# Kernel tuning notes

Measured on AMD Instinct MI355X. Metric: run time of the kernel, lower is better.

## Reference

```python
import jax, jax.numpy as jnp
import numpy as np

N, E, F_IN, F_OUT = 8192, 1024, 256, 256


def setup_inputs() -> dict:
    key = jax.random.key(0)
    k1, k2, k3, k4 = jax.random.split(key, 4)
    X = jax.random.normal(k1, (N, F_IN), dtype=jnp.float32)
    # binary incidence matrix: node i belongs to hyperedge j with p=0.05
    H = (jax.random.uniform(k2, (N, E)) < 0.05).astype(jnp.float32)
    W = jax.random.normal(k3, (F_OUT, F_IN), dtype=jnp.float32) * (1.0 / np.sqrt(F_IN))
    b = jax.random.normal(k4, (F_OUT,), dtype=jnp.float32) * 0.01
    return {"X": X, "H": H, "W": W, "b": b}


def reference(X, H, W, b):
    # Dv = diag(row sums of H), De = diag(col sums of H)
    dv = jnp.sum(H, axis=1)                      # [N] node degrees
    de = jnp.sum(H, axis=0)                      # [E] edge degrees
    dv_inv_sqrt = 1.0 / jnp.sqrt(dv)             # inv of sqrt(Dv) (diagonal)
    de_inv = 1.0 / de                            # inv of De (diagonal)
    # diagonal matrices realized as broadcast scalings (same math, no N x N).
    Xs = X * dv_inv_sqrt[:, None]
    M = H.T @ Xs                                 # H^T (...)          [E, F]
    M = M * de_inv[:, None]                      # De^-1 (...)        [E, F]
    X_new = (H @ M) * dv_inv_sqrt[:, None]       # Dv^-1/2 H (...)    [N, F]
    return X_new @ W.T + b                       # nn.Linear
```

## Files before the change

### kernel.cpp

```cpp
#include <hip/hip_runtime.h>
#include <hip/hip_bf16.h>
#include <stdint.h>

typedef __attribute__((ext_vector_type(8))) short bf16x8;
typedef __attribute__((ext_vector_type(4))) float f32x4;
typedef __attribute__((ext_vector_type(4))) unsigned int u32x4;
typedef __attribute__((ext_vector_type(2))) unsigned int u32x2;
typedef unsigned short u16;
typedef unsigned int u32;
typedef unsigned char u8;
typedef unsigned long long u64;

#define N_NODES 8192
#define N_EDGES 1024
#define F_DIM   256

__device__ __forceinline__ u16 f2bf(float f) {
    union { float f; u32 u; } v; v.f = f;
    u32 u = v.u;
    u = (u + 0x7FFFu + ((u >> 16) & 1u)) >> 16;
    return (u16)u;
}

__device__ __forceinline__ void async16(const u16* g, u16* l) {
    __builtin_amdgcn_global_load_lds(
        (const __attribute__((address_space(1))) u32*)(const void*)g,
        (__attribute__((address_space(3))) u32*)(void*)l, 16, 0, 0);
}

__device__ __forceinline__ bf16x8 expand8(u32 byte) {
    union { u32 u[4]; bf16x8 v; } r;
#pragma unroll
    for (int i = 0; i < 4; ++i)
        r.u[i] = (((byte >> (2 * i)) & 1u) ? 0x3F80u : 0u)
               | (((byte >> (2 * i + 1)) & 1u) ? 0x3F800000u : 0u);
    return r.v;
}

__global__ __launch_bounds__(512) void prep(
    const float* __restrict__ H, const float* __restrict__ X,
    const float* __restrict__ W,
    float* __restrict__ dv, u32* __restrict__ HbTs, u32* __restrict__ HbN,
    u16* __restrict__ Zt) {
    __shared__ u16 hmask[32][68];
    __shared__ u16 Xls[32][264];
    const int tid = threadIdx.x;
    const int wv = tid >> 6;
    const int lane = tid & 63;
    const int blk = blockIdx.x;
    const int n0 = blk * 32 + wv * 4;

    f32x4 hv[4][4], xv[4];
#pragma unroll
    for (int r = 0; r < 4; ++r) {
        const int n = n0 + r;
#pragma unroll
        for (int q = 0; q < 4; ++q)
            hv[r][q] = *(const f32x4*)(&H[(size_t)n * N_EDGES + q * 256 + lane * 4]);
        xv[r] = *(const f32x4*)(&X[(size_t)n * F_DIM + lane * 4]);
    }

#pragma unroll
    for (int r = 0; r < 4; ++r) {
        const int n = n0 + r;
        u32 m16 = 0u;
#pragma unroll
        for (int q = 0; q < 4; ++q)
#pragma unroll
            for (int j = 0; j < 4; ++j)
                m16 |= ((hv[r][q][j] != 0.f) ? 1u : 0u) << (q * 4 + j);
        hmask[wv * 4 + r][lane] = (u16)m16;
        u32 s = (u32)__popc(m16);
#pragma unroll
        for (int d = 1; d < 64; d <<= 1) s += __shfl_xor(s, d, 64);
        if (lane == 0) dv[n] = (float)s;
        const float sc = rsqrtf((float)s);
        u32x2 pk;
        pk[0] = (u32)f2bf(xv[r][0] * sc) | ((u32)f2bf(xv[r][1] * sc) << 16);
        pk[1] = (u32)f2bf(xv[r][2] * sc) | ((u32)f2bf(xv[r][3] * sc) << 16);
        *(u32x2*)(&Xls[wv * 4 + r][lane * 4]) = pk;
    }
    __syncthreads();
    {
        u32x2 st;
#pragma unroll
        for (int eo = 0; eo < 2; ++eo) {
            const int e = tid * 2 + eo;
            const int widx = (e & 255) >> 2;
            const int bit = ((e >> 8) << 2) + (e & 3);
            u32 w = 0u;
#pragma unroll
            for (int r = 0; r < 32; ++r)
                w |= (u32)((hmask[r][widx] >> bit) & 1u) << r;
            st[eo] = w;
        }
        *(u32x2*)(&HbTs[(size_t)blk * N_EDGES + tid * 2]) = st;
    }
    {
        const int r = tid & 31;
        const int wec = tid >> 5;
#pragma unroll
        for (int wo = 0; wo < 2; ++wo) {
            const int we = wec + wo * 16;
            const int q = we >> 3, l0 = (we & 7) * 8;
            const u32x2 a = *(const u32x2*)(&hmask[r][l0]);
            const u32x2 b2 = *(const u32x2*)(&hmask[r][l0 + 4]);
            const u32 sh = q * 4;
            u32 w = ((a[0] >> sh) & 0xFu)
                  | (((a[0] >> (16 + sh)) & 0xFu) << 4)
                  | (((a[1] >> sh) & 0xFu) << 8)
                  | (((a[1] >> (16 + sh)) & 0xFu) << 12)
                  | (((b2[0] >> sh) & 0xFu) << 16)
                  | (((b2[0] >> (16 + sh)) & 0xFu) << 20)
                  | (((b2[1] >> sh) & 0xFu) << 24)
                  | (((b2[1] >> (16 + sh)) & 0xFu) << 28);
            HbN[(size_t)we * N_NODES + blk * 32 + r] = w;
        }
    }
    {
        const int row16 = lane & 15, quad = lane >> 4;
        f32x4 acc[2][2] = {};
#pragma unroll
        for (int ks = 0; ks < 8; ++ks) {
            bf16x8 af[2];
#pragma unroll
            for (int tm = 0; tm < 2; ++tm)
                af[tm] = *(const bf16x8*)(&Xls[tm * 16 + row16][ks * 32 + quad * 8]);
#pragma unroll
            for (int tn = 0; tn < 2; ++tn) {
                const int j = wv * 32 + tn * 16 + row16;
                const f32x4 w0 = *(const f32x4*)(&W[(size_t)j * F_DIM + ks * 32 + quad * 8]);
                const f32x4 w1 = *(const f32x4*)(&W[(size_t)j * F_DIM + ks * 32 + quad * 8 + 4]);
                union { u32x4 u; bf16x8 v; } bu;
                bu.u[0] = (u32)f2bf(w0[0]) | ((u32)f2bf(w0[1]) << 16);
                bu.u[1] = (u32)f2bf(w0[2]) | ((u32)f2bf(w0[3]) << 16);
                bu.u[2] = (u32)f2bf(w1[0]) | ((u32)f2bf(w1[1]) << 16);
                bu.u[3] = (u32)f2bf(w1[2]) | ((u32)f2bf(w1[3]) << 16);
#pragma unroll
                for (int tm = 0; tm < 2; ++tm)
                    acc[tm][tn] = __builtin_amdgcn_mfma_f32_16x16x32_bf16(
                        af[tm], bu.v, acc[tm][tn], 0, 0, 0);
            }
        }
#pragma unroll
        for (int tm = 0; tm < 2; ++tm)
#pragma unroll
            for (int tn = 0; tn < 2; ++tn) {
                const int j = wv * 32 + tn * 16 + row16;
                u32x2 pk;
                pk[0] = (u32)f2bf(acc[tm][tn][0]) | ((u32)f2bf(acc[tm][tn][1]) << 16);
                pk[1] = (u32)f2bf(acc[tm][tn][2]) | ((u32)f2bf(acc[tm][tn][3]) << 16);
                *(u32x2*)(&Zt[(size_t)j * N_NODES + blk * 32 + tm * 16 + quad * 4]) = pk;
            }
    }
}

__global__ __launch_bounds__(512) void gemmM2(
    const u16* __restrict__ Zt, const u32* __restrict__ HbTs,
    u16* __restrict__ M2t) {
    __shared__ __align__(16) u8 smem[65536];
    __shared__ float cnts[8][2][16];
    const int tid = threadIdx.x;
    const int wv = tid >> 6, lane = tid & 63;
    const int f0 = ((int)blockIdx.x & 7) * 32;
    const int e0 = ((int)blockIdx.x >> 3) * 32;
    const int row16 = lane & 15, quad = lane >> 4;
    const int srow = lane & 15, schunk = lane >> 4;
    u16* myBs = (u16*)(smem + wv * 8192);
    const int kbase = wv * 1024;

    f32x4 acc[2][2] = {};
    u32 cnt0 = 0, cnt1 = 0;
    u32 wA[2][2], wB[2][2];

    auto STAGE = [&](int it, int buf) {
        __builtin_amdgcn_sched_barrier(0);
        const int k0 = kbase + it * 64;
#pragma unroll
        for (int tn = 0; tn < 2; ++tn)
#pragma unroll
            for (int ks = 0; ks < 2; ++ks)
                async16(Zt + (size_t)(f0 + tn * 16 + srow) * N_NODES + k0 + ks * 32 + schunk * 8,
                        myBs + buf * 2048 + (tn * 2 + ks) * 512);
    };
    auto LOADW = [&](int it, u32 (&w)[2][2]) {
        const int k0 = kbase + it * 64;
#pragma unroll
        for (int tm = 0; tm < 2; ++tm)
#pragma unroll
            for (int ks = 0; ks < 2; ++ks)
                w[tm][ks] = HbTs[(size_t)((k0 >> 5) + ks) * N_EDGES + e0 + tm * 16 + row16];
    };
    auto COMPUTE = [&](int buf, u32 (&w)[2][2]) {
        asm volatile("s_waitcnt vmcnt(4)" ::: "memory");
        __builtin_amdgcn_sched_barrier(0);
#pragma unroll
        for (int ks = 0; ks < 2; ++ks) {
            bf16x8 bfr[2];
#pragma unroll
            for (int tn = 0; tn < 2; ++tn)
                bfr[tn] = *(const bf16x8*)(myBs + buf * 2048 + (tn * 2 + ks) * 512 + lane * 8);
#pragma unroll
            for (int tm = 0; tm < 2; ++tm) {
                const u32 byte = (w[tm][ks] >> (quad * 8)) & 0xFFu;
                if (tm == 0) cnt0 += (u32)__popc(byte); else cnt1 += (u32)__popc(byte);
                const bf16x8 af = expand8(byte);
#pragma unroll
                for (int tn = 0; tn < 2; ++tn)
                    acc[tm][tn] = __builtin_amdgcn_mfma_f32_16x16x32_bf16(
                        af, bfr[tn], acc[tm][tn], 0, 0, 0);
            }
        }
    };

    STAGE(0, 0);
    LOADW(0, wA);
    for (int i = 0; i < 8; ++i) {
        STAGE(2 * i + 1, 1);
        LOADW(2 * i + 1, wB);
        COMPUTE(0, wA);
        const int nxt = (2 * i + 2 < 16) ? (2 * i + 2) : 15;
        STAGE(nxt, 0);
        LOADW(nxt, wA);
        COMPUTE(1, wB);
    }

    cnt0 += __shfl_down(cnt0, 32, 64); cnt0 += __shfl_down(cnt0, 16, 64);
    cnt1 += __shfl_down(cnt1, 32, 64); cnt1 += __shfl_down(cnt1, 16, 64);
    if (lane < 16) {
        cnts[wv][0][lane] = (float)cnt0;
        cnts[wv][1][lane] = (float)cnt1;
    }
    __syncthreads();
    {
        float* redf = (float*)smem;
        float* my = &redf[(size_t)(wv * 64 + lane) * 17];
#pragma unroll
        for (int tm = 0; tm < 2; ++tm)
#pragma unroll
            for (int tn = 0; tn < 2; ++tn)
#pragma unroll
                for (int r = 0; r < 4; ++r)
                    my[tm * 8 + tn * 4 + r] = acc[tm][tn][r];
    }
    __syncthreads();
    {
        const float* redf = (const float*)smem;
#pragma unroll
        for (int h = 0; h < 2; ++h) {
            const int idx = tid + h * 512;
            const int fl = idx >> 5, el = idx & 31;
            const int tm = el >> 4, q = (el >> 2) & 3, r = el & 3;
            const int tn = fl >> 4, r16 = fl & 15;
            const int srcl = q * 16 + r16;
            const int j = tm * 8 + tn * 4 + r;
            float s = 0.f, de = 0.f;
#pragma unroll
            for (int w = 0; w < 8; ++w) {
                s += redf[(size_t)(w * 64 + srcl) * 17 + j];
                de += cnts[w][tm][el & 15];
            }
            M2t[(size_t)(f0 + fl) * N_EDGES + e0 + el] = f2bf(s / de);
        }
    }
}

__global__ __launch_bounds__(512) void gemmOUT(
    const u16* __restrict__ M2t, const u32* __restrict__ HbN,
    const float* __restrict__ dv, const float* __restrict__ bias,
    float* __restrict__ out) {
    __shared__ __align__(16) u16 Bs[32 * 1028];
    const int tid = threadIdx.x;
    const int wv = tid >> 6, lane = tid & 63;
    const int row16 = lane & 15, quad = lane >> 4;
    const int j0 = ((int)blockIdx.x & 7) * 32;
    const int ng = ((int)blockIdx.x >> 3) * 256 + wv * 32;

#pragma unroll
    for (int rr = 0; rr < 4; ++rr) {
        const int jr = wv * 4 + rr;
#pragma unroll
        for (int c = 0; c < 2; ++c)
            async16(M2t + (size_t)(j0 + jr) * N_EDGES + c * 512 + lane * 8,
                    &Bs[jr * 1028 + c * 512]);
    }
    __syncthreads();

    f32x4 acc[2][2] = {};
    u32 wA[2][2], wB[2][2];
    auto LOADW = [&](int it, u32 (&w)[2][2]) {
#pragma unroll
        for (int tm = 0; tm < 2; ++tm)
#pragma unroll
            for (int ks = 0; ks < 2; ++ks)
                w[tm][ks] = HbN[(size_t)(it * 2 + ks) * N_NODES + ng + tm * 16 + row16];
    };
    auto COMPUTE = [&](int it, u32 (&w)[2][2]) {
#pragma unroll
        for (int ks = 0; ks < 2; ++ks) {
            bf16x8 bfr[2];
#pragma unroll
            for (int tn = 0; tn < 2; ++tn) {
                const int base = (tn * 16 + row16) * 1028 + it * 64 + ks * 32 + quad * 8;
                union { u32x2 lo_hi[2]; bf16x8 v; } u;
                u.lo_hi[0] = *(const u32x2*)(&Bs[base]);
                u.lo_hi[1] = *(const u32x2*)(&Bs[base + 4]);
                bfr[tn] = u.v;
            }
#pragma unroll
            for (int tm = 0; tm < 2; ++tm) {
                const u32 byte = (w[tm][ks] >> (quad * 8)) & 0xFFu;
                const bf16x8 af = expand8(byte);
#pragma unroll
                for (int tn = 0; tn < 2; ++tn)
                    acc[tm][tn] = __builtin_amdgcn_mfma_f32_16x16x32_bf16(
                        af, bfr[tn], acc[tm][tn], 0, 0, 0);
            }
        }
    };

    LOADW(0, wA);
    for (int i = 0; i < 8; ++i) {
        LOADW(2 * i + 1, wB);
        COMPUTE(2 * i, wA);
        const int nxt = (2 * i + 2 < 16) ? (2 * i + 2) : 15;
        LOADW(nxt, wA);
        COMPUTE(2 * i + 1, wB);
    }

#pragma unroll
    for (int tm = 0; tm < 2; ++tm)
#pragma unroll
        for (int tn = 0; tn < 2; ++tn) {
            const int col = j0 + tn * 16 + row16;
            const float bc = bias[col];
#pragma unroll
            for (int r = 0; r < 4; ++r) {
                const int n = ng + tm * 16 + quad * 4 + r;
                out[(size_t)n * F_DIM + col] = acc[tm][tn][r] * rsqrtf(dv[n]) + bc;
            }
        }
}

extern "C" void kernel_launch(void* const* d_in, const int* in_sizes, int n_in,
                              void* d_out, int out_size, void* d_ws, size_t ws_size,
                              hipStream_t stream) {
    (void)in_sizes; (void)n_in; (void)out_size; (void)ws_size;
    const float* X = (const float*)d_in[0];
    const float* H = (const float*)d_in[1];
    const float* W = (const float*)d_in[2];
    const float* b = (const float*)d_in[3];
    float* out = (float*)d_out;

    char* ws = (char*)d_ws;
    float* dv   = (float*)(ws);
    u32*   HbTs = (u32*)(ws + 0x10000);
    u32*   HbN  = (u32*)(ws + 0x110000);
    u16*   Zt   = (u16*)(ws + 0x210000);
    u16*   M2t  = (u16*)(ws + 0x610000);

    prep<<<256, 512, 0, stream>>>(H, X, W, dv, HbTs, HbN, Zt);
    gemmM2<<<256, 512, 0, stream>>>(Zt, HbTs, M2t);
    gemmOUT<<<256, 512, 0, stream>>>(M2t, HbN, dv, b, out);
}
```

Measured before the change: 122.3 us.

## Double prep block size to 1024 threads and relax gemmM2 async wait depth

```diff
diff --git a/kernel.cpp b/kernel.cpp
--- a/kernel.cpp
+++ b/kernel.cpp
@@ -37,7 +37,7 @@
     return r.v;
 }
 
-__global__ __launch_bounds__(512) void prep(
+__global__ __launch_bounds__(1024) void prep(
     const float* __restrict__ H, const float* __restrict__ X,
     const float* __restrict__ W,
     float* __restrict__ dv, u32* __restrict__ HbTs, u32* __restrict__ HbN,
@@ -48,11 +48,11 @@
     const int wv = tid >> 6;
     const int lane = tid & 63;
     const int blk = blockIdx.x;
-    const int n0 = blk * 32 + wv * 4;
-
-    f32x4 hv[4][4], xv[4];
-#pragma unroll
-    for (int r = 0; r < 4; ++r) {
+    const int n0 = blk * 32 + wv * 2;
+
+    f32x4 hv[2][4], xv[2];
+#pragma unroll
+    for (int r = 0; r < 2; ++r) {
         const int n = n0 + r;
 #pragma unroll
         for (int q = 0; q < 4; ++q)
@@ -61,7 +61,7 @@
     }
 
 #pragma unroll
-    for (int r = 0; r < 4; ++r) {
+    for (int r = 0; r < 2; ++r) {
         const int n = n0 + r;
         u32 m16 = 0u;
 #pragma unroll
@@ -69,7 +69,7 @@
 #pragma unroll
             for (int j = 0; j < 4; ++j)
                 m16 |= ((hv[r][q][j] != 0.f) ? 1u : 0u) << (q * 4 + j);
-        hmask[wv * 4 + r][lane] = (u16)m16;
+        hmask[wv * 2 + r][lane] = (u16)m16;
         u32 s = (u32)__popc(m16);
 #pragma unroll
         for (int d = 1; d < 64; d <<= 1) s += __shfl_xor(s, d, 64);
@@ -78,80 +78,65 @@
         u32x2 pk;
         pk[0] = (u32)f2bf(xv[r][0] * sc) | ((u32)f2bf(xv[r][1] * sc) << 16);
         pk[1] = (u32)f2bf(xv[r][2] * sc) | ((u32)f2bf(xv[r][3] * sc) << 16);
-        *(u32x2*)(&Xls[wv * 4 + r][lane * 4]) = pk;
+        *(u32x2*)(&Xls[wv * 2 + r][lane * 4]) = pk;
     }
     __syncthreads();
     {
-        u32x2 st;
-#pragma unroll
-        for (int eo = 0; eo < 2; ++eo) {
-            const int e = tid * 2 + eo;
-            const int widx = (e & 255) >> 2;
-            const int bit = ((e >> 8) << 2) + (e & 3);
-            u32 w = 0u;
-#pragma unroll
-            for (int r = 0; r < 32; ++r)
-                w |= (u32)((hmask[r][widx] >> bit) & 1u) << r;
-            st[eo] = w;
-        }
-        *(u32x2*)(&HbTs[(size_t)blk * N_EDGES + tid * 2]) = st;
+        const int e = tid;
+        const int widx = (e & 255) >> 2;
+        const int bit = ((e >> 8) << 2) + (e & 3);
+        u32 w = 0u;
+#pragma unroll
+        for (int r = 0; r < 32; ++r)
+            w |= (u32)((hmask[r][widx] >> bit) & 1u) << r;
+        HbTs[(size_t)blk * N_EDGES + e] = w;
     }
     {
         const int r = tid & 31;
-        const int wec = tid >> 5;
-#pragma unroll
-        for (int wo = 0; wo < 2; ++wo) {
-            const int we = wec + wo * 16;
-            const int q = we >> 3, l0 = (we & 7) * 8;
-            const u32x2 a = *(const u32x2*)(&hmask[r][l0]);
-            const u32x2 b2 = *(const u32x2*)(&hmask[r][l0 + 4]);
-            const u32 sh = q * 4;
-            u32 w = ((a[0] >> sh) & 0xFu)
-                  | (((a[0] >> (16 + sh)) & 0xFu) << 4)
-                  | (((a[1] >> sh) & 0xFu) << 8)
-                  | (((a[1] >> (16 + sh)) & 0xFu) << 12)
-                  | (((b2[0] >> sh) & 0xFu) << 16)
-                  | (((b2[0] >> (16 + sh)) & 0xFu) << 20)
-                  | (((b2[1] >> sh) & 0xFu) << 24)
-                  | (((b2[1] >> (16 + sh)) & 0xFu) << 28);
-            HbN[(size_t)we * N_NODES + blk * 32 + r] = w;
-        }
+        const int we = tid >> 5;
+        const int q = we >> 3, l0 = (we & 7) * 8;
+        const u32x2 a = *(const u32x2*)(&hmask[r][l0]);
+        const u32x2 b2 = *(const u32x2*)(&hmask[r][l0 + 4]);
+        const u32 sh = q * 4;
+        u32 w = ((a[0] >> sh) & 0xFu)
+              | (((a[0] >> (16 + sh)) & 0xFu) << 4)
+              | (((a[1] >> sh) & 0xFu) << 8)
+              | (((a[1] >> (16 + sh)) & 0xFu) << 12)
+              | (((b2[0] >> sh) & 0xFu) << 16)
+              | (((b2[0] >> (16 + sh)) & 0xFu) << 20)
+              | (((b2[1] >> sh) & 0xFu) << 24)
+              | (((b2[1] >> (16 + sh)) & 0xFu) << 28);
+        HbN[(size_t)we * N_NODES + blk * 32 + r] = w;
     }
     {
         const int row16 = lane & 15, quad = lane >> 4;
-        f32x4 acc[2][2] = {};
+        const int j = wv * 16 + row16;
+        f32x4 acc[2] = {};
 #pragma unroll
         for (int ks = 0; ks < 8; ++ks) {
             bf16x8 af[2];
 #pragma unroll
             for (int tm = 0; tm < 2; ++tm)
                 af[tm] = *(const bf16x8*)(&Xls[tm * 16 + row16][ks * 32 + quad * 8]);
-#pragma unroll
-            for (int tn = 0; tn < 2; ++tn) {
-                const int j = wv * 32 + tn * 16 + row16;
-                const f32x4 w0 = *(const f32x4*)(&W[(size_t)j * F_DIM + ks * 32 + quad * 8]);
-                const f32x4 w1 = *(const f32x4*)(&W[(size_t)j * F_DIM + ks * 32 + quad * 8 + 4]);
-                union { u32x4 u; bf16x8 v; } bu;
-                bu.u[0] = (u32)f2bf(w0[0]) | ((u32)f2bf(w0[1]) << 16);
-                bu.u[1] = (u32)f2bf(w0[2]) | ((u32)f2bf(w0[3]) << 16);
-                bu.u[2] = (u32)f2bf(w1[0]) | ((u32)f2bf(w1[1]) << 16);
-                bu.u[3] = (u32)f2bf(w1[2]) | ((u32)f2bf(w1[3]) << 16);
-#pragma unroll
-                for (int tm = 0; tm < 2; ++tm)
-                    acc[tm][tn] = __builtin_amdgcn_mfma_f32_16x16x32_bf16(
-                        af[tm], bu.v, acc[tm][tn], 0, 0, 0);
-            }
-        }
-#pragma unroll
-        for (int tm = 0; tm < 2; ++tm)
-#pragma unroll
-            for (int tn = 0; tn < 2; ++tn) {
-                const int j = wv * 32 + tn * 16 + row16;
-                u32x2 pk;
-                pk[0] = (u32)f2bf(acc[tm][tn][0]) | ((u32)f2bf(acc[tm][tn][1]) << 16);
-                pk[1] = (u32)f2bf(acc[tm][tn][2]) | ((u32)f2bf(acc[tm][tn][3]) << 16);
-                *(u32x2*)(&Zt[(size_t)j * N_NODES + blk * 32 + tm * 16 + quad * 4]) = pk;
-            }
+            const f32x4 w0 = *(const f32x4*)(&W[(size_t)j * F_DIM + ks * 32 + quad * 8]);
+            const f32x4 w1 = *(const f32x4*)(&W[(size_t)j * F_DIM + ks * 32 + quad * 8 + 4]);
+            union { u32x4 u; bf16x8 v; } bu;
+            bu.u[0] = (u32)f2bf(w0[0]) | ((u32)f2bf(w0[1]) << 16);
+            bu.u[1] = (u32)f2bf(w0[2]) | ((u32)f2bf(w0[3]) << 16);
+            bu.u[2] = (u32)f2bf(w1[0]) | ((u32)f2bf(w1[1]) << 16);
+            bu.u[3] = (u32)f2bf(w1[2]) | ((u32)f2bf(w1[3]) << 16);
+#pragma unroll
+            for (int tm = 0; tm < 2; ++tm)
+                acc[tm] = __builtin_amdgcn_mfma_f32_16x16x32_bf16(
+                    af[tm], bu.v, acc[tm], 0, 0, 0);
+        }
+#pragma unroll
+        for (int tm = 0; tm < 2; ++tm) {
+            u32x2 pk;
+            pk[0] = (u32)f2bf(acc[tm][0]) | ((u32)f2bf(acc[tm][1]) << 16);
+            pk[1] = (u32)f2bf(acc[tm][2]) | ((u32)f2bf(acc[tm][3]) << 16);
+            *(u32x2*)(&Zt[(size_t)j * N_NODES + blk * 32 + tm * 16 + quad * 4]) = pk;
+        }
     }
 }
 
@@ -192,7 +177,7 @@
                 w[tm][ks] = HbTs[(size_t)((k0 >> 5) + ks) * N_EDGES + e0 + tm * 16 + row16];
     };
     auto COMPUTE = [&](int buf, u32 (&w)[2][2]) {
-        asm volatile("s_waitcnt vmcnt(4)" ::: "memory");
+        asm volatile("s_waitcnt vmcnt(8)" ::: "memory");
         __builtin_amdgcn_sched_barrier(0);
 #pragma unroll
         for (int ks = 0; ks < 2; ++ks) {
@@ -359,7 +344,7 @@
     u16*   Zt   = (u16*)(ws + 0x210000);
     u16*   M2t  = (u16*)(ws + 0x610000);
 
-    prep<<<256, 512, 0, stream>>>(H, X, W, dv, HbTs, HbN, Zt);
+    prep<<<256, 1024, 0, stream>>>(H, X, W, dv, HbTs, HbN, Zt);
     gemmM2<<<256, 512, 0, stream>>>(Zt, HbTs, M2t);
     gemmOUT<<<256, 512, 0, stream>>>(M2t, HbN, dv, b, out);
 }
```

Measured after the change: 122.1 us. Within noise of the previous version (-0.2%).
